# Kernel optimization log

Measured on AMD Instinct MI355X. Metric: run time of the kernel, lower is better.

## Reference

```python
import jax, jax.numpy as jnp
import numpy as np

N, E, G = 50000, 600000, 512
F_IN, H, OUT = 128, 128, 256


def setup_inputs() -> dict:
    key = jax.random.key(0)
    ks = jax.random.split(key, 16)
    x = jax.random.normal(ks[0], (N, F_IN), dtype=jnp.float32)
    edge_index = jax.random.randint(ks[1], (2, E), 0, N, dtype=jnp.int64)
    batch = jnp.sort(jax.random.randint(ks[2], (N,), 0, G, dtype=jnp.int64))
    def lin(k, out_d, in_d):
        s = 1.0 / np.sqrt(in_d)
        return jax.random.uniform(k, (out_d, in_d), jnp.float32, -s, s)
    W1l, W1r = lin(ks[3], H, F_IN), lin(ks[4], H, F_IN)
    b1 = jnp.zeros((H,), jnp.float32)
    W2l, W2r = lin(ks[5], H, H), lin(ks[6], H, H)
    b2 = jnp.zeros((H,), jnp.float32)
    W3l, W3r = lin(ks[7], H, H), lin(ks[8], H, H)
    b3 = jnp.zeros((H,), jnp.float32)
    Wlin = lin(ks[9], OUT, 2 * H)
    blin = jnp.zeros((OUT,), jnp.float32)
    return dict(x=x, edge_index=edge_index, batch=batch,
                W1l=W1l, b1=b1, W1r=W1r, W2l=W2l, b2=b2, W2r=W2r,
                W3l=W3l, b3=b3, W3r=W3r, Wlin=Wlin, blin=blin)


def reference(x, edge_index, batch, W1l, b1, W1r, W2l, b2, W2r, W3l, b3, W3r, Wlin, blin):
    src, dst = edge_index[0], edge_index[1]
    # in-degree of each target node (mean aggregation denominator)
    deg = jax.ops.segment_sum(jnp.ones((E,), x.dtype), dst, num_segments=N)
    deg = jnp.maximum(deg, 1.0)[:, None]

    def sage(h, Wl, bl, Wr):
        # mean-aggregate neighbor features then linear; plus root transform
        agg = jax.ops.segment_sum(h[src], dst, num_segments=N) / deg
        return agg @ Wl.T + bl + h @ Wr.T

    h = jax.nn.relu(sage(x, W1l, b1, W1r))
    h = jax.nn.relu(sage(h, W2l, b2, W2r))
    h = sage(h, W3l, b3, W3r)

    # global max / mean pool per graph
    x_max = jax.ops.segment_max(h, batch, num_segments=G)
    x_max = jnp.where(jnp.isfinite(x_max), x_max, 0.0)
    cnt = jnp.maximum(jax.ops.segment_sum(jnp.ones((N,), h.dtype), batch, num_segments=G), 1.0)
    x_mean = jax.ops.segment_sum(h, batch, num_segments=G) / cnt[:, None]

    pooled = jnp.concatenate([x_max, x_mean], axis=1)  # [G, 2H]
    # dropout is identity in eval mode
    return pooled @ Wlin.T + blin
```

## Files before the change

### kernel.cpp

```cpp
#include <hip/hip_runtime.h>
#include <hip/hip_bf16.h>
#include <hip/hip_fp16.h>


#define FH 128
#define OUTD 256
#define SCHUNK 2048

typedef unsigned int u32;
typedef unsigned short u16;
typedef __attribute__((ext_vector_type(8))) _Float16 f16frag;
typedef __attribute__((ext_vector_type(4))) float f4frag;

__global__ void hist_kernel(const int* __restrict__ dst, int* __restrict__ cnt, int E) {
    int e = blockIdx.x * 256 + threadIdx.x;
    if (e < E) atomicAdd(&cnt[dst[e]], 1);
}

__global__ void scanA_kernel(const int* __restrict__ cnt, int* __restrict__ bsum, int n) {
    __shared__ int ws[4];
    int b = blockIdx.x, t = threadIdx.x;
    int base = b * SCHUNK + t * 8;
    int s = 0;
    #pragma unroll
    for (int k = 0; k < 8; ++k) {
        int i = base + k;
        s += (i < n) ? cnt[i] : 0;
    }
    #pragma unroll
    for (int off = 32; off >= 1; off >>= 1) s += __shfl_xor(s, off, 64);
    int w = t >> 6, lane = t & 63;
    if (lane == 0) ws[w] = s;
    __syncthreads();
    if (t == 0) bsum[b] = ws[0] + ws[1] + ws[2] + ws[3];
}

__global__ void scanB_kernel(const int* __restrict__ bsum, int* __restrict__ boff,
                             int* __restrict__ rp, int B, int n) {
    int t = threadIdx.x;
    int v = (t < B) ? bsum[t] : 0;
    int x = v;
    #pragma unroll
    for (int off = 1; off < 64; off <<= 1) {
        int y = __shfl_up(x, off, 64);
        if (t >= off) x += y;
    }
    if (t < B) boff[t] = x - v;
    if (t == 63) rp[n] = x;
}

__global__ void scanC_kernel(const int* __restrict__ cnt, const int* __restrict__ boff,
                             int* __restrict__ rp, float* __restrict__ dinv, int n) {
    __shared__ int ws[4];
    int b = blockIdx.x, t = threadIdx.x;
    int base = b * SCHUNK + t * 8;
    int v[8];
    int ts = 0;
    #pragma unroll
    for (int k = 0; k < 8; ++k) {
        int i = base + k;
        v[k] = (i < n) ? cnt[i] : 0;
        ts += v[k];
    }
    int w = t >> 6, lane = t & 63;
    int x = ts;
    #pragma unroll
    for (int off = 1; off < 64; off <<= 1) {
        int y = __shfl_up(x, off, 64);
        if (lane >= off) x += y;
    }
    if (lane == 63) ws[w] = x;
    __syncthreads();
    int woff = 0;
    #pragma unroll
    for (int q = 0; q < 4; ++q) woff += (q < w) ? ws[q] : 0;
    int run = boff[b] + woff + (x - ts);
    #pragma unroll
    for (int k = 0; k < 8; ++k) {
        int i = base + k;
        if (i < n) {
            rp[i] = run;
            dinv[i] = 1.0f / (float)max(v[k], 1);
        }
        run += v[k];
    }
}

__global__ void scatter_kernel(const int* __restrict__ src, const int* __restrict__ dst,
                               const int* __restrict__ rp, int* __restrict__ cursor,
                               int* __restrict__ esrc, int E) {
    int e = blockIdx.x * 256 + threadIdx.x;
    if (e < E) {
        int d = dst[e];
        int pos = rp[d] + atomicAdd(&cursor[d], 1);
        esrc[pos] = src[e];
    }
}

__global__ void graph_bounds_kernel(const int* __restrict__ batch, int* __restrict__ gstart,
                                    int n, int g) {
    int i = blockIdx.x * 256 + threadIdx.x;
    if (i >= n) return;
    int b = batch[i];
    int pb = (i == 0) ? -1 : batch[i - 1];
    for (int q = pb + 1; q <= b; ++q) gstart[q] = i;
    if (i == n - 1) {
        for (int q = b + 1; q <= g; ++q) gstart[q] = n;
    }
}

__global__ void prep_x(const float* __restrict__ x, u16* __restrict__ x16, int n4) {
    int id = blockIdx.x * 256 + threadIdx.x;
    if (id >= n4) return;
    float4 v = *(const float4*)(x + (size_t)id * 4);
    __half h0 = __float2half(v.x), h1 = __float2half(v.y);
    __half h2 = __float2half(v.z), h3 = __float2half(v.w);
    ushort4 s;
    s.x = *(u16*)&h0; s.y = *(u16*)&h1; s.z = *(u16*)&h2; s.w = *(u16*)&h3;
    *(ushort4*)(x16 + (size_t)id * 4) = s;
}

__global__ void prep_w(const float* __restrict__ W0, const float* __restrict__ W1,
                       const float* __restrict__ W2, const float* __restrict__ W3,
                       const float* __restrict__ W4, const float* __restrict__ W5,
                       uint4* __restrict__ Bf) {
    const float* Ws[6] = {W0, W1, W2, W3, W4, W5};
    int ks = blockIdx.x;
    int arr = blockIdx.y;
    int l = threadIdx.x;
    const float* W = Ws[arr];
    bool use_lo = (ks >= 4);
    int kb = (ks & 3) * 32 + (l >> 4) * 8;
    uint4* out = Bf + (size_t)arr * 4096;
    #pragma unroll
    for (int ot = 0; ot < 8; ++ot) {
        int o = ot * 16 + (l & 15);
        u32 h[8];
        #pragma unroll
        for (int i = 0; i < 8; ++i) {
            float v = W[o * 128 + kb + i];
            __half hi = __float2half(v);
            if (use_lo) {
                float rem = v - __half2float(hi);
                __half lo = __float2half(rem);
                h[i] = *(u16*)&lo;
            } else {
                h[i] = *(u16*)&hi;
            }
        }
        uint4 u;
        u.x = h[0] | (h[1] << 16);
        u.y = h[2] | (h[3] << 16);
        u.z = h[4] | (h[5] << 16);
        u.w = h[6] | (h[7] << 16);
        out[(ks * 8 + ot) * 64 + l] = u;
    }
}

__device__ inline void add8(float* a, uint4 u) {
    float2 f0 = __half22float2(*(__half2*)&u.x);
    float2 f1 = __half22float2(*(__half2*)&u.y);
    float2 f2 = __half22float2(*(__half2*)&u.z);
    float2 f3 = __half22float2(*(__half2*)&u.w);
    a[0] += f0.x; a[1] += f0.y; a[2] += f1.x; a[3] += f1.y;
    a[4] += f2.x; a[5] += f2.y; a[6] += f3.x; a[7] += f3.y;
}

__global__ void agg_kernel(const u16* __restrict__ h16,
                           const int* __restrict__ rp, const int* __restrict__ esrc,
                           const float* __restrict__ dinv,
                           u16* __restrict__ agg16, int n_nodes) {
    int node = blockIdx.x * 16 + (threadIdx.x >> 4);
    if (node >= n_nodes) return;
    int lane = threadIdx.x & 15;
    int f = lane * 8;
    int s0 = rp[node], s1 = rp[node + 1];
    float a0[8] = {0, 0, 0, 0, 0, 0, 0, 0};
    float a1[8] = {0, 0, 0, 0, 0, 0, 0, 0};
    float a2[8] = {0, 0, 0, 0, 0, 0, 0, 0};
    float a3[8] = {0, 0, 0, 0, 0, 0, 0, 0};
    int j = s0;
    for (; j + 4 <= s1; j += 4) {
        int i0 = esrc[j], i1 = esrc[j + 1], i2 = esrc[j + 2], i3 = esrc[j + 3];
        uint4 u0 = *(const uint4*)(h16 + (size_t)i0 * FH + f);
        uint4 u1 = *(const uint4*)(h16 + (size_t)i1 * FH + f);
        uint4 u2 = *(const uint4*)(h16 + (size_t)i2 * FH + f);
        uint4 u3 = *(const uint4*)(h16 + (size_t)i3 * FH + f);
        add8(a0, u0); add8(a1, u1); add8(a2, u2); add8(a3, u3);
    }
    for (; j < s1; ++j) {
        uint4 u0 = *(const uint4*)(h16 + (size_t)esrc[j] * FH + f);
        add8(a0, u0);
    }
    float di = dinv[node];
    u32 oh[8];
    #pragma unroll
    for (int i = 0; i < 8; ++i) {
        __half hv = __float2half((a0[i] + a1[i] + a2[i] + a3[i]) * di);
        oh[i] = *(u16*)&hv;
    }
    uint4 w;
    w.x = oh[0] | (oh[1] << 16);
    w.y = oh[2] | (oh[3] << 16);
    w.z = oh[4] | (oh[5] << 16);
    w.w = oh[6] | (oh[7] << 16);
    *(uint4*)(agg16 + (size_t)node * FH + f) = w;
}

__global__ __launch_bounds__(256, 2)
void mfma_gemm(const u16* __restrict__ A1, const u16* __restrict__ A2,
               const uint4* __restrict__ Bf1, const uint4* __restrict__ Bf2,
               const float* __restrict__ bias, u16* __restrict__ out16,
               int do_relu) {
    __shared__ uint4 Bl[4096];
    int tid = threadIdx.x;
    int l = tid & 63;
    int wv = tid >> 6;
    int bn0 = blockIdx.x * 192 + wv * 48;
    int m = l & 15, q = l >> 4;

    f4frag acc[3][8];
    #pragma unroll
    for (int i = 0; i < 3; ++i)
        #pragma unroll
        for (int o = 0; o < 8; ++o)
            acc[i][o] = (f4frag){0.f, 0.f, 0.f, 0.f};

    #pragma unroll
    for (int p = 0; p < 2; ++p) {
        const u16* P = p ? A2 : A1;
        const uint4* Bf = p ? Bf2 : Bf1;

        __syncthreads();

        uint4 tmp[16];
        #pragma unroll
        for (int u = 0; u < 16; ++u)
            tmp[u] = Bf[u * 256 + tid];
        f16frag Af[3][4];
        #pragma unroll
        for (int nt = 0; nt < 3; ++nt)
            #pragma unroll
            for (int s = 0; s < 4; ++s)
                Af[nt][s] = *(const f16frag*)(P + (size_t)(bn0 + nt * 16 + m) * FH + s * 32 + q * 8);
        #pragma unroll
        for (int u = 0; u < 16; ++u)
            Bl[u * 256 + tid] = tmp[u];
        __syncthreads();

        #pragma unroll
        for (int s = 0; s < 4; ++s) {
            f16frag Bhi[8], Blo[8];
            #pragma unroll
            for (int ot = 0; ot < 8; ++ot) {
                Bhi[ot] = *(const f16frag*)&Bl[(size_t)((s)     * 8 + ot) * 64 + l];
                Blo[ot] = *(const f16frag*)&Bl[(size_t)((s + 4) * 8 + ot) * 64 + l];
            }
            #pragma unroll
            for (int ot = 0; ot < 8; ++ot)
                #pragma unroll
                for (int nt = 0; nt < 3; ++nt)
                    acc[nt][ot] = __builtin_amdgcn_mfma_f32_16x16x32_f16(Af[nt][s], Bhi[ot], acc[nt][ot], 0, 0, 0);
            #pragma unroll
            for (int ot = 0; ot < 8; ++ot)
                #pragma unroll
                for (int nt = 0; nt < 3; ++nt)
                    acc[nt][ot] = __builtin_amdgcn_mfma_f32_16x16x32_f16(Af[nt][s], Blo[ot], acc[nt][ot], 0, 0, 0);
        }
    }

    #pragma unroll
    for (int nt = 0; nt < 3; ++nt)
        #pragma unroll
        for (int r = 0; r < 4; ++r) {
            int node = bn0 + nt * 16 + q * 4 + r;
            #pragma unroll
            for (int ot = 0; ot < 8; ++ot) {
                float v = acc[nt][ot][r] + bias[ot * 16 + m];
                if (do_relu) v = fmaxf(v, 0.f);
                __half hv = __float2half(v);
                out16[(size_t)node * FH + ot * 16 + m] = *(u16*)&hv;
            }
        }
}

__global__ __launch_bounds__(256, 2)
void pool_final(const u16* __restrict__ h16, const int* __restrict__ gstart,
                const float* __restrict__ Wlin, const float* __restrict__ blin,
                float* __restrict__ out) {
    __shared__ float smax[16][FH];
    __shared__ float ssum[16][FH];
    __shared__ float pr[2 * FH];
    int g = blockIdx.x;
    int tid = threadIdx.x;
    int way = tid >> 4;
    int lane = tid & 15;
    int f = lane * 8;
    int s = gstart[g], e = gstart[g + 1];

    float mx[8], sm[8];
    #pragma unroll
    for (int i = 0; i < 8; ++i) { mx[i] = -INFINITY; sm[i] = 0.f; }
    for (int n = s + way; n < e; n += 16) {
        uint4 u = *(const uint4*)(h16 + (size_t)n * FH + f);
        float2 f0 = __half22float2(*(__half2*)&u.x);
        float2 f1 = __half22float2(*(__half2*)&u.y);
        float2 f2 = __half22float2(*(__half2*)&u.z);
        float2 f3 = __half22float2(*(__half2*)&u.w);
        float v[8] = {f0.x, f0.y, f1.x, f1.y, f2.x, f2.y, f3.x, f3.y};
        #pragma unroll
        for (int i = 0; i < 8; ++i) {
            mx[i] = fmaxf(mx[i], v[i]);
            sm[i] += v[i];
        }
    }
    #pragma unroll
    for (int i = 0; i < 8; ++i) {
        smax[way][f + i] = mx[i];
        ssum[way][f + i] = sm[i];
    }
    __syncthreads();
    int c = e - s;
    if (tid < FH) {
        float m2 = -INFINITY, s2 = 0.f;
        #pragma unroll
        for (int w2 = 0; w2 < 16; ++w2) {
            m2 = fmaxf(m2, smax[w2][tid]);
            s2 += ssum[w2][tid];
        }
        pr[tid] = (c > 0) ? m2 : 0.f;
        pr[FH + tid] = s2 / (float)max(c, 1);
    }
    __syncthreads();
    int o = tid;
    const float4* wr = (const float4*)(Wlin + (size_t)o * (2 * FH));
    float acc = 0.f;
    #pragma unroll
    for (int j = 0; j < (2 * FH) / 4; ++j) {
        float4 wv = wr[j];
        acc += wv.x * pr[j * 4 + 0] + wv.y * pr[j * 4 + 1] +
               wv.z * pr[j * 4 + 2] + wv.w * pr[j * 4 + 3];
    }
    out[(size_t)g * OUTD + o] = acc + blin[o];
}

extern "C" void kernel_launch(void* const* d_in, const int* in_sizes, int n_in,
                              void* d_out, int out_size, void* d_ws, size_t ws_size,
                              hipStream_t stream) {
    const float* x     = (const float*)d_in[0];
    const int*   ei    = (const int*)d_in[1];
    const int*   batch = (const int*)d_in[2];
    const float* W1l = (const float*)d_in[3];
    const float* b1  = (const float*)d_in[4];
    const float* W1r = (const float*)d_in[5];
    const float* W2l = (const float*)d_in[6];
    const float* b2  = (const float*)d_in[7];
    const float* W2r = (const float*)d_in[8];
    const float* W3l = (const float*)d_in[9];
    const float* b3  = (const float*)d_in[10];
    const float* W3r = (const float*)d_in[11];
    const float* Wlin = (const float*)d_in[12];
    const float* blin = (const float*)d_in[13];
    float* out = (float*)d_out;

    const int E = in_sizes[1] / 2;
    const int N = in_sizes[2];
    const int G = out_size / OUTD;
    const int* src = ei;
    const int* dst = ei + E;
    const int NB = (N + SCHUNK - 1) / SCHUNK;
    const int GB = (N + 191) / 192;
    const int NP = GB * 192;

    char* w = (char*)d_ws;
    auto alloc = [&](size_t bytes) {
        void* p = (void*)w;
        w += (bytes + 255) & ~(size_t)255;
        return p;
    };
    int*   cnt    = (int*)alloc((size_t)2 * N * sizeof(int));
    int*   cursor = cnt + N;
    int*   rp     = (int*)alloc((size_t)(N + 1) * sizeof(int));
    int*   esrc   = (int*)alloc((size_t)E * sizeof(int));
    int*   gstart = (int*)alloc((size_t)(G + 1) * sizeof(int));
    float* dinv   = (float*)alloc((size_t)N * sizeof(float));
    int*   bsum   = (int*)alloc(64 * sizeof(int));
    int*   boff   = (int*)alloc(64 * sizeof(int));
    u16*   x16    = (u16*)alloc((size_t)NP * FH * sizeof(u16));
    u16*   agg16  = (u16*)alloc((size_t)NP * FH * sizeof(u16));
    u16*   hA16   = (u16*)alloc((size_t)NP * FH * sizeof(u16));
    u16*   hB16   = (u16*)alloc((size_t)NP * FH * sizeof(u16));
    uint4* BF     = (uint4*)alloc((size_t)6 * 4096 * sizeof(uint4));
    (void)ws_size;

    prep_x<<<(N * 32 + 255) / 256, 256, 0, stream>>>(x, x16, N * 32);
    prep_w<<<dim3(8, 6), 64, 0, stream>>>(W1l, W1r, W2l, W2r, W3l, W3r, BF);

    hipMemsetAsync(cnt, 0, (size_t)2 * N * sizeof(int), stream);
    hist_kernel<<<(E + 255) / 256, 256, 0, stream>>>(dst, cnt, E);
    scanA_kernel<<<NB, 256, 0, stream>>>(cnt, bsum, N);
    scanB_kernel<<<1, 64, 0, stream>>>(bsum, boff, rp, NB, N);
    scanC_kernel<<<NB, 256, 0, stream>>>(cnt, boff, rp, dinv, N);
    scatter_kernel<<<(E + 255) / 256, 256, 0, stream>>>(src, dst, rp, cursor, esrc, E);
    graph_bounds_kernel<<<(N + 255) / 256, 256, 0, stream>>>(batch, gstart, N, G);

    const int agg_grid = (N + 15) / 16;

    agg_kernel<<<agg_grid, 256, 0, stream>>>(x16, rp, esrc, dinv, agg16, N);
    mfma_gemm<<<GB, 256, 0, stream>>>(agg16, x16, BF + 0 * 4096, BF + 1 * 4096, b1, hA16, 1);
    agg_kernel<<<agg_grid, 256, 0, stream>>>(hA16, rp, esrc, dinv, agg16, N);
    mfma_gemm<<<GB, 256, 0, stream>>>(agg16, hA16, BF + 2 * 4096, BF + 3 * 4096, b2, hB16, 1);
    agg_kernel<<<agg_grid, 256, 0, stream>>>(hB16, rp, esrc, dinv, agg16, N);
    mfma_gemm<<<GB, 256, 0, stream>>>(agg16, hB16, BF + 4 * 4096, BF + 5 * 4096, b3, hA16, 0);

    pool_final<<<G, 256, 0, stream>>>(hA16, gstart, Wlin, blin, out);
}
```

Before: 343.2 us.

## Merge preprocessing kernels, fold scan, unroll gather by 8, drop LDS in GEMM

Combines prep_x, prep_w and the degree histogram into one launch, folds the single-block offset scan into scanC, and merges the CSR scatter with graph-bound computation. This cuts the number of small kernel launches and their serialization gaps. The aggregation loop is unrolled to 8 neighbors to keep more gathers in flight. The GEMM becomes single-wave blocks of 48 rows that read B fragments straight from global/L2 instead of staging them in LDS, which raises redundant B traffic but removes barriers.

```diff
diff --git a/kernel.cpp b/kernel.cpp
--- a/kernel.cpp
+++ b/kernel.cpp
@@ -12,9 +12,60 @@
 typedef __attribute__((ext_vector_type(8))) _Float16 f16frag;
 typedef __attribute__((ext_vector_type(4))) float f4frag;
 
-__global__ void hist_kernel(const int* __restrict__ dst, int* __restrict__ cnt, int E) {
-    int e = blockIdx.x * 256 + threadIdx.x;
-    if (e < E) atomicAdd(&cnt[dst[e]], 1);
+__global__ void prep_all(const float* __restrict__ x, u16* __restrict__ x16, int n4, int PX,
+                         const float* __restrict__ W0, const float* __restrict__ W1,
+                         const float* __restrict__ W2, const float* __restrict__ W3,
+                         const float* __restrict__ W4, const float* __restrict__ W5,
+                         uint4* __restrict__ Bf, int PW,
+                         const int* __restrict__ dst, int* __restrict__ cnt, int E) {
+    int blk = blockIdx.x;
+    if (blk < PX) {
+        int id = blk * 256 + threadIdx.x;
+        if (id >= n4) return;
+        float4 v = *(const float4*)(x + (size_t)id * 4);
+        __half h0 = __float2half(v.x), h1 = __float2half(v.y);
+        __half h2 = __float2half(v.z), h3 = __float2half(v.w);
+        ushort4 s;
+        s.x = *(u16*)&h0; s.y = *(u16*)&h1; s.z = *(u16*)&h2; s.w = *(u16*)&h3;
+        *(ushort4*)(x16 + (size_t)id * 4) = s;
+    } else if (blk < PX + PW) {
+        int pair = (blk - PX) * 4 + (threadIdx.x >> 6);
+        if (pair >= 48) return;
+        int ks = pair & 7;
+        int arr = pair >> 3;
+        int l = threadIdx.x & 63;
+        const float* Ws[6] = {W0, W1, W2, W3, W4, W5};
+        const float* W = Ws[arr];
+        bool use_lo = (ks >= 4);
+        int kb = (ks & 3) * 32 + (l >> 4) * 8;
+        uint4* out = Bf + (size_t)arr * 4096;
+        #pragma unroll
+        for (int ot = 0; ot < 8; ++ot) {
+            int o = ot * 16 + (l & 15);
+            u32 h[8];
+            #pragma unroll
+            for (int i = 0; i < 8; ++i) {
+                float v = W[o * 128 + kb + i];
+                __half hi = __float2half(v);
+                if (use_lo) {
+                    float rem = v - __half2float(hi);
+                    __half lo = __float2half(rem);
+                    h[i] = *(u16*)&lo;
+                } else {
+                    h[i] = *(u16*)&hi;
+                }
+            }
+            uint4 u;
+            u.x = h[0] | (h[1] << 16);
+            u.y = h[2] | (h[3] << 16);
+            u.z = h[4] | (h[5] << 16);
+            u.w = h[6] | (h[7] << 16);
+            out[(ks * 8 + ot) * 64 + l] = u;
+        }
+    } else {
+        int e = (blk - PX - PW) * 256 + threadIdx.x;
+        if (e < E) atomicAdd(&cnt[dst[e]], 1);
+    }
 }
 
 __global__ void scanA_kernel(const int* __restrict__ cnt, int* __restrict__ bsum, int n) {
@@ -35,24 +86,26 @@
     if (t == 0) bsum[b] = ws[0] + ws[1] + ws[2] + ws[3];
 }
 
-__global__ void scanB_kernel(const int* __restrict__ bsum, int* __restrict__ boff,
-                             int* __restrict__ rp, int B, int n) {
-    int t = threadIdx.x;
-    int v = (t < B) ? bsum[t] : 0;
-    int x = v;
-    #pragma unroll
-    for (int off = 1; off < 64; off <<= 1) {
-        int y = __shfl_up(x, off, 64);
-        if (t >= off) x += y;
-    }
-    if (t < B) boff[t] = x - v;
-    if (t == 63) rp[n] = x;
-}
-
-__global__ void scanC_kernel(const int* __restrict__ cnt, const int* __restrict__ boff,
-                             int* __restrict__ rp, float* __restrict__ dinv, int n) {
+__global__ void scanC_kernel(const int* __restrict__ cnt, const int* __restrict__ bsum,
+                             int NB, int* __restrict__ rp, float* __restrict__ dinv, int n) {
     __shared__ int ws[4];
+    __shared__ int base_s;
     int b = blockIdx.x, t = threadIdx.x;
+    if (t < 64) {
+        int v = (t < NB) ? bsum[t] : 0;
+        int pre = (t < b) ? v : 0;
+        #pragma unroll
+        for (int off = 32; off >= 1; off >>= 1) pre += __shfl_xor(pre, off, 64);
+        if (t == 0) base_s = pre;
+        if (b == 0) {
+            int tot = v;
+            #pragma unroll
+            for (int off = 32; off >= 1; off >>= 1) tot += __shfl_xor(tot, off, 64);
+            if (t == 0) rp[n] = tot;
+        }
+    }
+    __syncthreads();
+    int boff = base_s;
     int base = b * SCHUNK + t * 8;
     int v[8];
     int ts = 0;
@@ -74,7 +127,7 @@
     int woff = 0;
     #pragma unroll
     for (int q = 0; q < 4; ++q) woff += (q < w) ? ws[q] : 0;
-    int run = boff[b] + woff + (x - ts);
+    int run = boff + woff + (x - ts);
     #pragma unroll
     for (int k = 0; k < 8; ++k) {
         int i = base + k;
@@ -86,74 +139,28 @@
     }
 }
 
-__global__ void scatter_kernel(const int* __restrict__ src, const int* __restrict__ dst,
+__global__ void scatter_bounds(const int* __restrict__ src, const int* __restrict__ dst,
                                const int* __restrict__ rp, int* __restrict__ cursor,
-                               int* __restrict__ esrc, int E) {
-    int e = blockIdx.x * 256 + threadIdx.x;
-    if (e < E) {
-        int d = dst[e];
-        int pos = rp[d] + atomicAdd(&cursor[d], 1);
-        esrc[pos] = src[e];
-    }
-}
-
-__global__ void graph_bounds_kernel(const int* __restrict__ batch, int* __restrict__ gstart,
-                                    int n, int g) {
-    int i = blockIdx.x * 256 + threadIdx.x;
-    if (i >= n) return;
-    int b = batch[i];
-    int pb = (i == 0) ? -1 : batch[i - 1];
-    for (int q = pb + 1; q <= b; ++q) gstart[q] = i;
-    if (i == n - 1) {
-        for (int q = b + 1; q <= g; ++q) gstart[q] = n;
-    }
-}
-
-__global__ void prep_x(const float* __restrict__ x, u16* __restrict__ x16, int n4) {
-    int id = blockIdx.x * 256 + threadIdx.x;
-    if (id >= n4) return;
-    float4 v = *(const float4*)(x + (size_t)id * 4);
-    __half h0 = __float2half(v.x), h1 = __float2half(v.y);
-    __half h2 = __float2half(v.z), h3 = __float2half(v.w);
-    ushort4 s;
-    s.x = *(u16*)&h0; s.y = *(u16*)&h1; s.z = *(u16*)&h2; s.w = *(u16*)&h3;
-    *(ushort4*)(x16 + (size_t)id * 4) = s;
-}
-
-__global__ void prep_w(const float* __restrict__ W0, const float* __restrict__ W1,
-                       const float* __restrict__ W2, const float* __restrict__ W3,
-                       const float* __restrict__ W4, const float* __restrict__ W5,
-                       uint4* __restrict__ Bf) {
-    const float* Ws[6] = {W0, W1, W2, W3, W4, W5};
-    int ks = blockIdx.x;
-    int arr = blockIdx.y;
-    int l = threadIdx.x;
-    const float* W = Ws[arr];
-    bool use_lo = (ks >= 4);
-    int kb = (ks & 3) * 32 + (l >> 4) * 8;
-    uint4* out = Bf + (size_t)arr * 4096;
-    #pragma unroll
-    for (int ot = 0; ot < 8; ++ot) {
-        int o = ot * 16 + (l & 15);
-        u32 h[8];
-        #pragma unroll
-        for (int i = 0; i < 8; ++i) {
-            float v = W[o * 128 + kb + i];
-            __half hi = __float2half(v);
-            if (use_lo) {
-                float rem = v - __half2float(hi);
-                __half lo = __float2half(rem);
-                h[i] = *(u16*)&lo;
-            } else {
-                h[i] = *(u16*)&hi;
-            }
-        }
-        uint4 u;
-        u.x = h[0] | (h[1] << 16);
-        u.y = h[2] | (h[3] << 16);
-        u.z = h[4] | (h[5] << 16);
-        u.w = h[6] | (h[7] << 16);
-        out[(ks * 8 + ot) * 64 + l] = u;
+                               int* __restrict__ esrc, int E, int SC,
+                               const int* __restrict__ batch, int* __restrict__ gstart,
+                               int n, int g) {
+    int blk = blockIdx.x;
+    if (blk < SC) {
+        int e = blk * 256 + threadIdx.x;
+        if (e < E) {
+            int d = dst[e];
+            int pos = rp[d] + atomicAdd(&cursor[d], 1);
+            esrc[pos] = src[e];
+        }
+    } else {
+        int i = (blk - SC) * 256 + threadIdx.x;
+        if (i >= n) return;
+        int b = batch[i];
+        int pb = (i == 0) ? -1 : batch[i - 1];
+        for (int q = pb + 1; q <= b; ++q) gstart[q] = i;
+        if (i == n - 1) {
+            for (int q = b + 1; q <= g; ++q) gstart[q] = n;
+        }
     }
 }
 
@@ -180,13 +187,28 @@
     float a2[8] = {0, 0, 0, 0, 0, 0, 0, 0};
     float a3[8] = {0, 0, 0, 0, 0, 0, 0, 0};
     int j = s0;
-    for (; j + 4 <= s1; j += 4) {
+    for (; j + 8 <= s1; j += 8) {
+        int i0 = esrc[j],     i1 = esrc[j + 1], i2 = esrc[j + 2], i3 = esrc[j + 3];
+        int i4 = esrc[j + 4], i5 = esrc[j + 5], i6 = esrc[j + 6], i7 = esrc[j + 7];
+        uint4 u0 = *(const uint4*)(h16 + (size_t)i0 * FH + f);
+        uint4 u1 = *(const uint4*)(h16 + (size_t)i1 * FH + f);
+        uint4 u2 = *(const uint4*)(h16 + (size_t)i2 * FH + f);
+        uint4 u3 = *(const uint4*)(h16 + (size_t)i3 * FH + f);
+        uint4 u4 = *(const uint4*)(h16 + (size_t)i4 * FH + f);
+        uint4 u5 = *(const uint4*)(h16 + (size_t)i5 * FH + f);
+        uint4 u6 = *(const uint4*)(h16 + (size_t)i6 * FH + f);
+        uint4 u7 = *(const uint4*)(h16 + (size_t)i7 * FH + f);
+        add8(a0, u0); add8(a1, u1); add8(a2, u2); add8(a3, u3);
+        add8(a0, u4); add8(a1, u5); add8(a2, u6); add8(a3, u7);
+    }
+    if (j + 4 <= s1) {
         int i0 = esrc[j], i1 = esrc[j + 1], i2 = esrc[j + 2], i3 = esrc[j + 3];
         uint4 u0 = *(const uint4*)(h16 + (size_t)i0 * FH + f);
         uint4 u1 = *(const uint4*)(h16 + (size_t)i1 * FH + f);
         uint4 u2 = *(const uint4*)(h16 + (size_t)i2 * FH + f);
         uint4 u3 = *(const uint4*)(h16 + (size_t)i3 * FH + f);
         add8(a0, u0); add8(a1, u1); add8(a2, u2); add8(a3, u3);
+        j += 4;
     }
     for (; j < s1; ++j) {
         uint4 u0 = *(const uint4*)(h16 + (size_t)esrc[j] * FH + f);
@@ -207,16 +229,13 @@
     *(uint4*)(agg16 + (size_t)node * FH + f) = w;
 }
 
-__global__ __launch_bounds__(256, 2)
+__global__ __launch_bounds__(64, 2)
 void mfma_gemm(const u16* __restrict__ A1, const u16* __restrict__ A2,
                const uint4* __restrict__ Bf1, const uint4* __restrict__ Bf2,
                const float* __restrict__ bias, u16* __restrict__ out16,
                int do_relu) {
-    __shared__ uint4 Bl[4096];
-    int tid = threadIdx.x;
-    int l = tid & 63;
-    int wv = tid >> 6;
-    int bn0 = blockIdx.x * 192 + wv * 48;
+    int l = threadIdx.x;
+    int bn0 = blockIdx.x * 48;
     int m = l & 15, q = l >> 4;
 
     f4frag acc[3][8];
@@ -231,30 +250,22 @@
         const u16* P = p ? A2 : A1;
         const uint4* Bf = p ? Bf2 : Bf1;
 
-        __syncthreads();
-
-        uint4 tmp[16];
-        #pragma unroll
-        for (int u = 0; u < 16; ++u)
-            tmp[u] = Bf[u * 256 + tid];
         f16frag Af[3][4];
         #pragma unroll
         for (int nt = 0; nt < 3; ++nt)
             #pragma unroll
             for (int s = 0; s < 4; ++s)
                 Af[nt][s] = *(const f16frag*)(P + (size_t)(bn0 + nt * 16 + m) * FH + s * 32 + q * 8);
-        #pragma unroll
-        for (int u = 0; u < 16; ++u)
-            Bl[u * 256 + tid] = tmp[u];
-        __syncthreads();
 
         #pragma unroll
         for (int s = 0; s < 4; ++s) {
             f16frag Bhi[8], Blo[8];
             #pragma unroll
             for (int ot = 0; ot < 8; ++ot) {
-                Bhi[ot] = *(const f16frag*)&Bl[(size_t)((s)     * 8 + ot) * 64 + l];
-                Blo[ot] = *(const f16frag*)&Bl[(size_t)((s + 4) * 8 + ot) * 64 + l];
+                uint4 bh = Bf[(size_t)((s)     * 8 + ot) * 64 + l];
+                uint4 bl = Bf[(size_t)((s + 4) * 8 + ot) * 64 + l];
+                Bhi[ot] = *(f16frag*)&bh;
+                Blo[ot] = *(f16frag*)&bl;
             }
             #pragma unroll
             for (int ot = 0; ot < 8; ++ot)
@@ -369,8 +380,8 @@
     const int* src = ei;
     const int* dst = ei + E;
     const int NB = (N + SCHUNK - 1) / SCHUNK;
-    const int GB = (N + 191) / 192;
-    const int NP = GB * 192;
+    const int GB = (N + 47) / 48;
+    const int NP = GB * 48;
 
     char* w = (char*)d_ws;
     auto alloc = [&](size_t bytes) {
@@ -385,7 +396,6 @@
     int*   gstart = (int*)alloc((size_t)(G + 1) * sizeof(int));
     float* dinv   = (float*)alloc((size_t)N * sizeof(float));
     int*   bsum   = (int*)alloc(64 * sizeof(int));
-    int*   boff   = (int*)alloc(64 * sizeof(int));
     u16*   x16    = (u16*)alloc((size_t)NP * FH * sizeof(u16));
     u16*   agg16  = (u16*)alloc((size_t)NP * FH * sizeof(u16));
     u16*   hA16   = (u16*)alloc((size_t)NP * FH * sizeof(u16));
@@ -393,25 +403,30 @@
     uint4* BF     = (uint4*)alloc((size_t)6 * 4096 * sizeof(uint4));
     (void)ws_size;
 
-    prep_x<<<(N * 32 + 255) / 256, 256, 0, stream>>>(x, x16, N * 32);
-    prep_w<<<dim3(8, 6), 64, 0, stream>>>(W1l, W1r, W2l, W2r, W3l, W3r, BF);
-
     hipMemsetAsync(cnt, 0, (size_t)2 * N * sizeof(int), stream);
-    hist_kernel<<<(E + 255) / 256, 256, 0, stream>>>(dst, cnt, E);
+    const int n4 = N * 32;
+    const int PX = (n4 + 255) / 256;
+    const int PW = 12;
+    const int PH = (E + 255) / 256;
+    prep_all<<<PX + PW + PH, 256, 0, stream>>>(x, x16, n4, PX,
+                                               W1l, W1r, W2l, W2r, W3l, W3r, BF, PW,
+                                               dst, cnt, E);
+
     scanA_kernel<<<NB, 256, 0, stream>>>(cnt, bsum, N);
-    scanB_kernel<<<1, 64, 0, stream>>>(bsum, boff, rp, NB, N);
-    scanC_kernel<<<NB, 256, 0, stream>>>(cnt, boff, rp, dinv, N);
-    scatter_kernel<<<(E + 255) / 256, 256, 0, stream>>>(src, dst, rp, cursor, esrc, E);
-    graph_bounds_kernel<<<(N + 255) / 256, 256, 0, stream>>>(batch, gstart, N, G);
+    scanC_kernel<<<NB, 256, 0, stream>>>(cnt, bsum, NB, rp, dinv, N);
+    const int SC = (E + 255) / 256;
+    const int GBND = (N + 255) / 256;
+    scatter_bounds<<<SC + GBND, 256, 0, stream>>>(src, dst, rp, cursor, esrc, E, SC,
+                                                  batch, gstart, N, G);
 
     const int agg_grid = (N + 15) / 16;
 
     agg_kernel<<<agg_grid, 256, 0, stream>>>(x16, rp, esrc, dinv, agg16, N);
-    mfma_gemm<<<GB, 256, 0, stream>>>(agg16, x16, BF + 0 * 4096, BF + 1 * 4096, b1, hA16, 1);
+    mfma_gemm<<<GB, 64, 0, stream>>>(agg16, x16, BF + 0 * 4096, BF + 1 * 4096, b1, hA16, 1);
     agg_kernel<<<agg_grid, 256, 0, stream>>>(hA16, rp, esrc, dinv, agg16, N);
-    mfma_gemm<<<GB, 256, 0, stream>>>(agg16, hA16, BF + 2 * 4096, BF + 3 * 4096, b2, hB16, 1);
+    mfma_gemm<<<GB, 64, 0, stream>>>(agg16, hA16, BF + 2 * 4096, BF + 3 * 4096, b2, hB16, 1);
     agg_kernel<<<agg_grid, 256, 0, stream>>>(hB16, rp, esrc, dinv, agg16, N);
-    mfma_gemm<<<GB, 256, 0, stream>>>(agg16, hB16, BF + 4 * 4096, BF + 5 * 4096, b3, hA16, 0);
+    mfma_gemm<<<GB, 64, 0, stream>>>(agg16, hB16, BF + 4 * 4096, BF + 5 * 4096, b3, hA16, 0);
 
     pool_final<<<G, 256, 0, stream>>>(hA16, gstart, Wlin, blin, out);
 }
```

After: 368.1 us. 7.2% more time.
